# Kernel optimization log

Hardware: AMD Instinct MI355X
Metric: run time of the kernel (lower is better)

The kernel has to match this reference:

```python
import jax, jax.numpy as jnp
import numpy as np

N_STATE = 512   # n
N_CTRL = 128    # m
HORIZON = 256   # T


def setup_inputs() -> dict:
    key = jax.random.key(0)
    k1, k2, k3, k4 = jax.random.split(key, 4)
    dim = N_STATE + N_CTRL
    # F scaled for a stable backward Riccati recursion over HORIZON steps
    F = jax.random.normal(k1, (N_STATE, dim), jnp.float32) * (0.3 / np.sqrt(dim))
    f = jax.random.normal(k2, (N_STATE,), jnp.float32) * 0.1
    # SPD cost matrix so Q_uu is always invertible (positive definite)
    A = jax.random.normal(k3, (dim, dim), jnp.float32)
    C = A @ A.T / dim + jnp.eye(dim, dtype=jnp.float32)
    c = jax.random.normal(k4, (dim,), jnp.float32) * 0.1
    return {"F": F, "f": f, "C": C, "c": c, "T": HORIZON}


def reference(F, f, C, c, T):
    n = F.shape[0]  # state size
    # final value function: V = C_xx, v = c_x, const = 0
    V0 = C[:n, :n]
    v0 = c[:n]
    const0 = jnp.zeros((), C.dtype)

    def step(carry, _):
        V, v, const = carry
        # compute_Q
        FV = F.T @ V                 # [(n+m), n]
        Q = C + FV @ F               # [(n+m), (n+m)]
        q = c + FV @ f + F.T @ v     # [(n+m)]
        Quu = Q[n:, n:]
        Qux = Q[n:, :n]
        qu = q[n:]
        # compute_K
        inv_Quu = jnp.linalg.inv(Quu)
        K = -inv_Quu @ Qux           # [m, n]
        k = -inv_Quu @ qu            # [m]
        # compute_V
        Qxx = Q[:n, :n]
        Qxu = Q[:n, n:]
        qx = q[:n]
        KQuu = K.T @ Quu
        Vn = Qxx + Qxu @ K + K.T @ Qux + KQuu @ K
        vn = qx + Qxu @ k + K.T @ qu + KQuu @ k
        # compute_const (note: W in compute_W equals Q algebraically, so W_uu=Quu, w_u=qu)
        Vf = V @ f
        constn = const + 0.5 * (k @ (Quu @ k)) + k @ qu + 0.5 * (f @ Vf) + f @ v
        return (Vn, vn, constn), (K, k, Vn, vn, constn)

    _, ys = jax.lax.scan(step, (V0, v0, const0), None, length=T)
    Ks, ks, Vs, vs, consts = ys
    # original inserts at front each iteration -> reverse time axis;
    # value_fn[:-1] drops the final (terminal) V, i.e. keeps exactly the T step outputs
    rev = lambda a: a[::-1]
    return (rev(Ks), rev(ks), rev(Vs), rev(vs), rev(consts))
```

## Files before the change

### kernel.cpp

```cpp
#include <hip/hip_runtime.h>
#include <math.h>

#define N_ST 512
#define N_CT 128
#define DIM  640
#define T_H  256
#define LTRI 8256

__global__ __launch_bounds__(256) void gemm_tn(
    const float* __restrict__ A, int lda,
    const float* __restrict__ B, int ldb,
    const float* __restrict__ Cs, int ldc,
    float* __restrict__ D, int ldd,
    int K, float alpha)
{
  __shared__ float As[16][34];
  __shared__ float Bs[16][68];
  const int tid = threadIdx.x;
  const int tx = tid & 15, ty = tid >> 4;
  const int i0 = blockIdx.x * 32, j0 = blockIdx.y * 64;
  const int iiA = tid & 31, kkA = tid >> 5;
  const int jjB = tid & 63, kkB = tid >> 6;
  float acc[2][4] = {};
  for (int k0 = 0; k0 < K; k0 += 16) {
    As[kkA][iiA]   = A[(size_t)(k0 + kkA) * lda + i0 + iiA];
    As[kkA+8][iiA] = A[(size_t)(k0 + kkA + 8) * lda + i0 + iiA];
#pragma unroll
    for (int r = 0; r < 4; r++)
      Bs[kkB + 4*r][jjB] = B[(size_t)(k0 + kkB + 4*r) * ldb + j0 + jjB];
    __syncthreads();
#pragma unroll
    for (int kk = 0; kk < 16; kk++) {
      float a0 = As[kk][ty*2+0], a1 = As[kk][ty*2+1];
      float b0 = Bs[kk][tx*4+0], b1 = Bs[kk][tx*4+1];
      float b2 = Bs[kk][tx*4+2], b3 = Bs[kk][tx*4+3];
      acc[0][0] += a0*b0; acc[0][1] += a0*b1; acc[0][2] += a0*b2; acc[0][3] += a0*b3;
      acc[1][0] += a1*b0; acc[1][1] += a1*b1; acc[1][2] += a1*b2; acc[1][3] += a1*b3;
    }
    __syncthreads();
  }
#pragma unroll
  for (int r = 0; r < 2; r++) {
    int i = i0 + ty*2 + r, j = j0 + tx*4;
    float4 o;
    o.x = alpha*acc[r][0]; o.y = alpha*acc[r][1];
    o.z = alpha*acc[r][2]; o.w = alpha*acc[r][3];
    if (Cs) {
      float4 c4 = *(const float4*)(Cs + (size_t)i*ldc + j);
      o.x += c4.x; o.y += c4.y; o.z += c4.z; o.w += c4.w;
    }
    *(float4*)(D + (size_t)i*ldd + j) = o;
  }
}

__global__ __launch_bounds__(256) void gemm_nn(
    const float* __restrict__ A, int lda,
    const float* __restrict__ B, int ldb,
    const float* __restrict__ Cs, int ldc,
    float* __restrict__ D, int ldd,
    int K)
{
  __shared__ float As[32][17];
  __shared__ float Bs[16][68];
  const int tid = threadIdx.x;
  const int tx = tid & 15, ty = tid >> 4;
  const int i0 = blockIdx.x * 32, j0 = blockIdx.y * 64;
  const int kkA = tid & 15, iiA = tid >> 4;
  const int jjB = tid & 63, kkB = tid >> 6;
  float acc[2][4] = {};
  for (int k0 = 0; k0 < K; k0 += 16) {
    As[iiA][kkA]     = A[(size_t)(i0 + iiA) * lda + k0 + kkA];
    As[iiA+16][kkA]  = A[(size_t)(i0 + iiA + 16) * lda + k0 + kkA];
#pragma unroll
    for (int r = 0; r < 4; r++)
      Bs[kkB + 4*r][jjB] = B[(size_t)(k0 + kkB + 4*r) * ldb + j0 + jjB];
    __syncthreads();
#pragma unroll
    for (int kk = 0; kk < 16; kk++) {
      float a0 = As[ty*2+0][kk], a1 = As[ty*2+1][kk];
      float b0 = Bs[kk][tx*4+0], b1 = Bs[kk][tx*4+1];
      float b2 = Bs[kk][tx*4+2], b3 = Bs[kk][tx*4+3];
      acc[0][0] += a0*b0; acc[0][1] += a0*b1; acc[0][2] += a0*b2; acc[0][3] += a0*b3;
      acc[1][0] += a1*b0; acc[1][1] += a1*b1; acc[1][2] += a1*b2; acc[1][3] += a1*b3;
    }
    __syncthreads();
  }
#pragma unroll
  for (int r = 0; r < 2; r++) {
    int i = i0 + ty*2 + r, j = j0 + tx*4;
    float4 c4 = *(const float4*)(Cs + (size_t)i*ldc + j);
    float4 o;
    o.x = c4.x + acc[r][0]; o.y = c4.y + acc[r][1];
    o.z = c4.z + acc[r][2]; o.w = c4.w + acc[r][3];
    *(float4*)(D + (size_t)i*ldd + j) = o;
  }
}

__global__ __launch_bounds__(1024) void combo_kernel(
    const float* __restrict__ Qm,
    const float* __restrict__ FV,
    const float* __restrict__ F,
    const float* __restrict__ f,
    const float* __restrict__ cvec,
    const float* __restrict__ vin,
    const float* __restrict__ Vin, int ldV,
    float* __restrict__ qv,
    float* __restrict__ Vf,
    float* __restrict__ fv,
    float* __restrict__ Lout,
    float* __restrict__ invd)
{
  __shared__ float Sp[LTRI];
  __shared__ float dinv[128];
  __shared__ float red[1024];
  const int tid = threadIdx.x;
  const int b = blockIdx.x;

  if (b == 0) {
    for (int idx = tid; idx < LTRI; idx += 1024) {
      int r = (int)((sqrtf(8.0f*idx + 1.0f) - 1.0f) * 0.5f);
      while ((r+1)*(r+2)/2 <= idx) r++;
      while (r*(r+1)/2 > idx) r--;
      int c = idx - r*(r+1)/2;
      Sp[idx] = Qm[(size_t)(N_ST + r)*DIM + N_ST + c];
    }
    __syncthreads();

    for (int p = 0; p < 128; p += 16) {
      if (tid < 64) {
        const int t = tid;
        const int toff = (p + t)*(p + t + 1)/2;
        float a[16];
#pragma unroll
        for (int c2 = 0; c2 < 16; c2++)
          a[c2] = (t < 16 && c2 <= t) ? Sp[toff + p + c2] : 0.0f;
        float Lr[16];
        float myinv = 0.0f;
#pragma unroll
        for (int j = 0; j < 16; j++) {
          float dj  = __shfl(a[j], j);
          float sq  = sqrtf(dj);
          float inv = 1.0f / sq;
          float Ltj = (t == j) ? sq : a[j] * inv;
#pragma unroll
          for (int jp = j + 1; jp < 16; jp++) {
            float Lpj = __shfl(Ltj, jp);
            a[jp] -= Ltj * Lpj;
          }
          Lr[j] = Ltj;
          if (t == j) myinv = inv;
        }
        if (t < 16) {
#pragma unroll
          for (int j = 0; j < 16; j++)
            if (j <= t) Sp[toff + p + j] = Lr[j];
          dinv[p + t] = myinv;
        }
      }
      __syncthreads();

      {
        int r = p + 16 + tid;
        if (r < 128) {
          const int roff = r*(r+1)/2;
          float Lrow[16];
#pragma unroll
          for (int jj = 0; jj < 16; jj++) {
            float accv = Sp[roff + p + jj];
            const int doff = (p + jj)*(p + jj + 1)/2;
#pragma unroll
            for (int t2 = 0; t2 < 16; t2++)
              if (t2 < jj) accv -= Lrow[t2] * Sp[doff + p + t2];
            Lrow[jj] = accv * dinv[p + jj];
          }
#pragma unroll
          for (int jj = 0; jj < 16; jj++) Sp[roff + p + jj] = Lrow[jj];
        }
      }
      __syncthreads();

      {
        int nR = 112 - p;
        if (nR > 0) {
          int nq = nR >> 2;
          int pairs = nq * (nq + 1) / 2;
          for (int e = tid; e < pairs; e += 1024) {
            int ri = (int)((sqrtf(8.0f*e + 1.0f) - 1.0f) * 0.5f);
            while ((ri+1)*(ri+2)/2 <= e) ri++;
            while (ri*(ri+1)/2 > e) ri--;
            int ci = e - ri*(ri+1)/2;
            int r0 = p + 16 + ri*4;
            int c0 = p + 16 + ci*4;
            bool dg = (ri == ci);
            int ro[4], co[4];
#pragma unroll
            for (int i2 = 0; i2 < 4; i2++) ro[i2] = (r0+i2)*(r0+i2+1)/2;
#pragma unroll
            for (int j2 = 0; j2 < 4; j2++) co[j2] = (c0+j2)*(c0+j2+1)/2;
            float acc[4][4];
#pragma unroll
            for (int i2 = 0; i2 < 4; i2++)
#pragma unroll
              for (int j2 = 0; j2 < 4; j2++)
                acc[i2][j2] = (!dg || (c0+j2) <= (r0+i2)) ? Sp[ro[i2] + c0 + j2] : 0.0f;
#pragma unroll
            for (int t2 = 0; t2 < 16; t2++) {
              float rv[4], cv2[4];
#pragma unroll
              for (int i2 = 0; i2 < 4; i2++) rv[i2]  = Sp[ro[i2] + p + t2];
#pragma unroll
              for (int j2 = 0; j2 < 4; j2++) cv2[j2] = Sp[co[j2] + p + t2];
#pragma unroll
              for (int i2 = 0; i2 < 4; i2++)
#pragma unroll
                for (int j2 = 0; j2 < 4; j2++)
                  acc[i2][j2] -= rv[i2] * cv2[j2];
            }
#pragma unroll
            for (int i2 = 0; i2 < 4; i2++)
#pragma unroll
              for (int j2 = 0; j2 < 4; j2++)
                if (!dg || (c0+j2) <= (r0+i2)) Sp[ro[i2] + c0 + j2] = acc[i2][j2];
          }
        }
      }
      __syncthreads();
    }

    for (int idx = tid; idx < LTRI; idx += 1024) Lout[idx] = Sp[idx];
    if (tid < 128) invd[tid] = dinv[tid];

  } else if (b == 1) {
    if (tid < DIM) {
      float acc = cvec[tid];
      const float4* fr = (const float4*)(FV + (size_t)tid * N_ST);
      const float4* f4 = (const float4*)f;
      float a4 = 0.0f;
      for (int kk = 0; kk < N_ST/4; kk++) {
        float4 x = fr[kk], y = f4[kk];
        a4 += x.x*y.x + x.y*y.y + x.z*y.z + x.w*y.w;
      }
      float a2 = 0.0f;
      for (int k = 0; k < N_ST; k++)
        a2 += F[(size_t)k*DIM + tid] * vin[k];
      qv[tid] = acc + a4 + a2;
    }
  } else {
    if (tid < N_ST) {
      const float4* vr = (const float4*)(Vin + (size_t)tid * ldV);
      const float4* f4 = (const float4*)f;
      float a4 = 0.0f;
      for (int kk = 0; kk < N_ST/4; kk++) {
        float4 x = vr[kk], y = f4[kk];
        a4 += x.x*y.x + x.y*y.y + x.z*y.z + x.w*y.w;
      }
      Vf[tid] = a4;
    }
    float pv = (tid < N_ST) ? f[tid] * vin[tid] : 0.0f;
    red[tid] = pv;
    __syncthreads();
    for (int s2 = 512; s2 > 0; s2 >>= 1) {
      if (tid < s2) red[tid] += red[tid + s2];
      __syncthreads();
    }
    if (tid == 0) *fv = red[0];
  }
}

__global__ __launch_bounds__(256) void trsm_kernel(
    const float* __restrict__ Lw,
    const float* __restrict__ invd,
    const float* __restrict__ Qm,
    const float* __restrict__ qv,
    float* __restrict__ W,
    float* __restrict__ wv,
    float* __restrict__ kv,
    float* __restrict__ outK,
    float* __restrict__ outks)
{
  __shared__ float Lp[LTRI];
  __shared__ float di[128];
  const int tid = threadIdx.x;
  for (int idx = tid; idx < LTRI; idx += 256) Lp[idx] = Lw[idx];
  if (tid < 128) di[tid] = invd[tid];
  __syncthreads();

  const int wvid = tid >> 6, lane = tid & 63;
  const int j = blockIdx.x * 4 + wvid;
  if (j > N_ST) return;

  float b0, b1;
  if (j < N_ST) {
    b0 = Qm[(size_t)(N_ST + lane)*DIM + j];
    b1 = Qm[(size_t)(N_ST + 64 + lane)*DIM + j];
  } else {
    b0 = qv[N_ST + lane];
    b1 = qv[N_ST + 64 + lane];
  }

  float x0 = 0.0f, x1 = 0.0f;
  int uoff = 0;
  for (int u = 0; u < 128; u++) {
    float s = Lp[uoff + lane]*x0 + Lp[uoff + 64 + lane]*x1;
#pragma unroll
    for (int off = 32; off > 0; off >>= 1) s += __shfl_xor(s, off);
    float bu = (u < 64) ? __shfl(b0, u) : __shfl(b1, u - 64);
    float wu = (bu - s) * di[u];
    if (u < 64) { if (lane == u)      x0 = wu; }
    else        { if (lane == u - 64) x1 = wu; }
    uoff += u + 1;
  }
  if (j < N_ST) {
    W[(size_t)lane*N_ST + j]        = x0;
    W[(size_t)(64 + lane)*N_ST + j] = x1;
  } else {
    wv[lane] = x0; wv[64 + lane] = x1;
  }

  const int toff0 = lane*(lane + 1)/2;
  const int toff1 = (64 + lane)*(65 + lane)/2;
  float y0 = 0.0f, y1 = 0.0f;
  for (int u = 127; u >= 0; u--) {
    float s = Lp[toff0 + u]*y0 + Lp[toff1 + u]*y1;
#pragma unroll
    for (int off = 32; off > 0; off >>= 1) s += __shfl_xor(s, off);
    float wu2 = (u < 64) ? __shfl(x0, u) : __shfl(x1, u - 64);
    float yu = (wu2 - s) * di[u];
    if (u < 64) { if (lane == u)      y0 = yu; }
    else        { if (lane == u - 64) y1 = yu; }
  }
  if (j < N_ST) {
    outK[(size_t)lane*N_ST + j]        = -y0;
    outK[(size_t)(64 + lane)*N_ST + j] = -y1;
  } else {
    kv[lane] = -y0; kv[64 + lane] = -y1;
    outks[lane] = -y0; outks[64 + lane] = -y1;
  }
}

__global__ __launch_bounds__(256) void finish_kernel(
    const float* __restrict__ Qm,
    const float* __restrict__ qv,
    const float* __restrict__ W,
    const float* __restrict__ wv,
    const float* __restrict__ kv,
    const float* __restrict__ Vf,
    const float* __restrict__ fv,
    const float* __restrict__ f,
    const float* __restrict__ constp,
    float* __restrict__ outV,
    float* __restrict__ outv,
    float* __restrict__ outc,
    float* __restrict__ wsconst)
{
  const int b = blockIdx.x, tid = threadIdx.x;
  if (b < 128) {
    __shared__ float As[16][34];
    __shared__ float Bs[16][68];
    const int tx = tid & 15, ty = tid >> 4;
    const int i0 = (b >> 3) * 32, j0 = (b & 7) * 64;
    const int iiA = tid & 31, kkA = tid >> 5;
    const int jjB = tid & 63, kkB = tid >> 6;
    float acc[2][4] = {};
    for (int k0 = 0; k0 < N_CT; k0 += 16) {
      As[kkA][iiA]   = W[(size_t)(k0 + kkA)*N_ST + i0 + iiA];
      As[kkA+8][iiA] = W[(size_t)(k0 + kkA + 8)*N_ST + i0 + iiA];
#pragma unroll
      for (int r = 0; r < 4; r++)
        Bs[kkB + 4*r][jjB] = W[(size_t)(k0 + kkB + 4*r)*N_ST + j0 + jjB];
      __syncthreads();
#pragma unroll
      for (int kk = 0; kk < 16; kk++) {
        float a0 = As[kk][ty*2+0], a1 = As[kk][ty*2+1];
        float b0v = Bs[kk][tx*4+0], b1v = Bs[kk][tx*4+1];
        float b2v = Bs[kk][tx*4+2], b3v = Bs[kk][tx*4+3];
        acc[0][0] += a0*b0v; acc[0][1] += a0*b1v; acc[0][2] += a0*b2v; acc[0][3] += a0*b3v;
        acc[1][0] += a1*b0v; acc[1][1] += a1*b1v; acc[1][2] += a1*b2v; acc[1][3] += a1*b3v;
      }
      __syncthreads();
    }
#pragma unroll
    for (int r = 0; r < 2; r++) {
      int i = i0 + ty*2 + r, j = j0 + tx*4;
      float4 qx = *(const float4*)(Qm + (size_t)i*DIM + j);
      float4 o;
      o.x = qx.x - acc[r][0]; o.y = qx.y - acc[r][1];
      o.z = qx.z - acc[r][2]; o.w = qx.w - acc[r][3];
      *(float4*)(outV + (size_t)i*N_ST + j) = o;
    }
  } else if (b < 136) {
    if (tid < 64) {
      int i = (b - 128)*64 + tid;
      float acc = 0.0f;
      for (int u = 0; u < N_CT; u++) acc += W[(size_t)u*N_ST + i] * wv[u];
      outv[i] = qv[i] - acc;
    }
  } else {
    __shared__ float red[256];
    float pv = 0.0f;
    if (tid < 128) {
      float qk = 0.0f;
      for (int u = 0; u < 128; u++)
        qk += Qm[(size_t)(N_ST + tid)*DIM + N_ST + u] * kv[u];
      pv = kv[tid] * (0.5f*qk + qv[N_ST + tid]);
      float fa = 0.0f;
#pragma unroll
      for (int r = 0; r < 4; r++) { int jj = tid*4 + r; fa += f[jj] * Vf[jj]; }
      pv += 0.5f * fa;
    }
    red[tid] = pv;
    __syncthreads();
    for (int s2 = 128; s2 > 0; s2 >>= 1) {
      if (tid < s2) red[tid] += red[tid + s2];
      __syncthreads();
    }
    if (tid == 0) {
      float cn = constp[0] + red[0] + fv[0];
      outc[0] = cn;
      wsconst[0] = cn;
    }
  }
}

extern "C" void kernel_launch(void* const* d_in, const int* in_sizes, int n_in,
                              void* d_out, int out_size, void* d_ws, size_t ws_size,
                              hipStream_t stream)
{
  (void)in_sizes; (void)n_in; (void)out_size; (void)ws_size;
  const float* F  = (const float*)d_in[0];
  const float* f  = (const float*)d_in[1];
  const float* Cm = (const float*)d_in[2];
  const float* cv = (const float*)d_in[3];

  float* out   = (float*)d_out;
  float* outK  = out;
  float* outks = outK  + (size_t)T_H * N_CT * N_ST;
  float* outVs = outks + (size_t)T_H * N_CT;
  float* outvs = outVs + (size_t)T_H * N_ST * N_ST;
  float* outcs = outvs + (size_t)T_H * N_ST;

  float* ws   = (float*)d_ws;
  float* FV   = ws;
  float* Qm   = FV   + (size_t)DIM * N_ST;
  float* qv   = Qm   + (size_t)DIM * DIM;
  float* Lw   = qv   + DIM;
  float* invd = Lw   + LTRI;
  float* W    = invd + N_CT;
  float* wv   = W    + (size_t)N_CT * N_ST;
  float* kv   = wv   + N_CT;
  float* Vf   = kv   + N_CT;
  float* fv   = Vf   + N_ST;
  float* cst  = fv   + 1;

  hipMemsetAsync(cst, 0, sizeof(float), stream);

  for (int s = 0; s < T_H; s++) {
    const float* Vin; int ldV; const float* vin;
    if (s == 0) { Vin = Cm; ldV = DIM; vin = cv; }
    else {
      Vin = outVs + (size_t)(T_H - s) * N_ST * N_ST; ldV = N_ST;
      vin = outvs + (size_t)(T_H - s) * N_ST;
    }
    const size_t slot = (size_t)(T_H - 1 - s);

    dim3 g1(DIM/32, N_ST/64);
    gemm_tn<<<g1, 256, 0, stream>>>(F, DIM, Vin, ldV, nullptr, 0, FV, N_ST,
                                    N_ST, 1.0f);
    dim3 g2(DIM/32, DIM/64);
    gemm_nn<<<g2, 256, 0, stream>>>(FV, N_ST, F, DIM, Cm, DIM, Qm, DIM, N_ST);
    combo_kernel<<<3, 1024, 0, stream>>>(Qm, FV, F, f, cv, vin, Vin, ldV,
                                         qv, Vf, fv, Lw, invd);
    trsm_kernel<<<129, 256, 0, stream>>>(Lw, invd, Qm, qv, W, wv, kv,
                                         outK + slot * N_CT * N_ST,
                                         outks + slot * N_CT);
    finish_kernel<<<137, 256, 0, stream>>>(Qm, qv, W, wv, kv, Vf, fv, f, cst,
                                           outVs + slot * N_ST * N_ST,
                                           outvs + slot * N_ST,
                                           outcs + slot, cst);
  }
}
```

Before: 56.59 ms.

## Use split-bf16 MFMA GEMMs for Riccati matrix products

Replaces the scalar FP32 tiled GEMMs (F^T V, FV F, and the V update W^T W) with one MFMA kernel. It emulates fp32 using a bf16 hi/lo split and three bf16 MFMAs per tile product. F^T is converted once up front, and each GEMM epilogue emits the bf16 hi/lo copies the next step consumes. W is now stored transposed so the update and the vector matvec read contiguous rows. Dropping the lo*lo term and using bf16 pieces may cost some accuracy over the 256-step recursion.

```diff
diff --git a/kernel.cpp b/kernel.cpp
--- a/kernel.cpp
+++ b/kernel.cpp
@@ -7,93 +7,120 @@
 #define T_H  256
 #define LTRI 8256
 
-__global__ __launch_bounds__(256) void gemm_tn(
-    const float* __restrict__ A, int lda,
-    const float* __restrict__ B, int ldb,
-    const float* __restrict__ Cs, int ldc,
+typedef __attribute__((ext_vector_type(8))) short bf16x8;
+typedef __attribute__((ext_vector_type(4))) float f32x4;
+
+__device__ __forceinline__ ushort f2bf(float x) {
+  unsigned u = __float_as_uint(x);
+  unsigned r = (u + 0x7fffu + ((u >> 16) & 1u)) >> 16;
+  return (ushort)r;
+}
+__device__ __forceinline__ float bf2f(ushort h) {
+  return __uint_as_float(((unsigned)h) << 16);
+}
+
+__global__ __launch_bounds__(256) void gemm_nt_mfma(
+    const ushort* __restrict__ Ah, const ushort* __restrict__ Al, int lda,
+    const ushort* __restrict__ Bh, const ushort* __restrict__ Bl, int ldb,
+    const float* __restrict__ Cs, int ldc, float beta,
     float* __restrict__ D, int ldd,
-    int K, float alpha)
-{
-  __shared__ float As[16][34];
-  __shared__ float Bs[16][68];
+    ushort* __restrict__ Dh, ushort* __restrict__ Dl,
+    int K)
+{
+  __shared__ ushort As_h[64*72], As_l[64*72], Bs_h[64*72], Bs_l[64*72];
   const int tid = threadIdx.x;
-  const int tx = tid & 15, ty = tid >> 4;
-  const int i0 = blockIdx.x * 32, j0 = blockIdx.y * 64;
-  const int iiA = tid & 31, kkA = tid >> 5;
-  const int jjB = tid & 63, kkB = tid >> 6;
-  float acc[2][4] = {};
-  for (int k0 = 0; k0 < K; k0 += 16) {
-    As[kkA][iiA]   = A[(size_t)(k0 + kkA) * lda + i0 + iiA];
-    As[kkA+8][iiA] = A[(size_t)(k0 + kkA + 8) * lda + i0 + iiA];
-#pragma unroll
-    for (int r = 0; r < 4; r++)
-      Bs[kkB + 4*r][jjB] = B[(size_t)(k0 + kkB + 4*r) * ldb + j0 + jjB];
+  const int i0 = blockIdx.x * 64, j0 = blockIdx.y * 64;
+  const int wid = tid >> 6, lane = tid & 63;
+  const int wm = (wid & 1) * 32, wn = (wid >> 1) * 32;
+  const int fr = lane & 15, fq = lane >> 4;
+
+  f32x4 acc[2][2];
+#pragma unroll
+  for (int a = 0; a < 2; a++)
+#pragma unroll
+    for (int b = 0; b < 2; b++) acc[a][b] = (f32x4){0.f, 0.f, 0.f, 0.f};
+
+  for (int k0 = 0; k0 < K; k0 += 64) {
+#pragma unroll
+    for (int h = 0; h < 2; h++) {
+      int c = tid + h * 256;
+      int row = c >> 3, col = (c & 7) << 3;
+      *(uint4*)&As_h[row*72 + col] = *(const uint4*)&Ah[(size_t)(i0+row)*lda + k0 + col];
+      *(uint4*)&As_l[row*72 + col] = *(const uint4*)&Al[(size_t)(i0+row)*lda + k0 + col];
+      *(uint4*)&Bs_h[row*72 + col] = *(const uint4*)&Bh[(size_t)(j0+row)*ldb + k0 + col];
+      *(uint4*)&Bs_l[row*72 + col] = *(const uint4*)&Bl[(size_t)(j0+row)*ldb + k0 + col];
+    }
     __syncthreads();
 #pragma unroll
-    for (int kk = 0; kk < 16; kk++) {
-      float a0 = As[kk][ty*2+0], a1 = As[kk][ty*2+1];
-      float b0 = Bs[kk][tx*4+0], b1 = Bs[kk][tx*4+1];
-      float b2 = Bs[kk][tx*4+2], b3 = Bs[kk][tx*4+3];
-      acc[0][0] += a0*b0; acc[0][1] += a0*b1; acc[0][2] += a0*b2; acc[0][3] += a0*b3;
-      acc[1][0] += a1*b0; acc[1][1] += a1*b1; acc[1][2] += a1*b2; acc[1][3] += a1*b3;
+    for (int kc = 0; kc < 64; kc += 32) {
+      bf16x8 ah[2], al[2], bh[2], bl[2];
+#pragma unroll
+      for (int t = 0; t < 2; t++) {
+        ah[t] = *(bf16x8*)&As_h[(wm + t*16 + fr)*72 + kc + fq*8];
+        al[t] = *(bf16x8*)&As_l[(wm + t*16 + fr)*72 + kc + fq*8];
+        bh[t] = *(bf16x8*)&Bs_h[(wn + t*16 + fr)*72 + kc + fq*8];
+        bl[t] = *(bf16x8*)&Bs_l[(wn + t*16 + fr)*72 + kc + fq*8];
+      }
+#pragma unroll
+      for (int tm = 0; tm < 2; tm++)
+#pragma unroll
+        for (int tn = 0; tn < 2; tn++) {
+          acc[tm][tn] = __builtin_amdgcn_mfma_f32_16x16x32_bf16(ah[tm], bh[tn], acc[tm][tn], 0, 0, 0);
+          acc[tm][tn] = __builtin_amdgcn_mfma_f32_16x16x32_bf16(ah[tm], bl[tn], acc[tm][tn], 0, 0, 0);
+          acc[tm][tn] = __builtin_amdgcn_mfma_f32_16x16x32_bf16(al[tm], bh[tn], acc[tm][tn], 0, 0, 0);
+        }
     }
     __syncthreads();
   }
-#pragma unroll
-  for (int r = 0; r < 2; r++) {
-    int i = i0 + ty*2 + r, j = j0 + tx*4;
-    float4 o;
-    o.x = alpha*acc[r][0]; o.y = alpha*acc[r][1];
-    o.z = alpha*acc[r][2]; o.w = alpha*acc[r][3];
-    if (Cs) {
-      float4 c4 = *(const float4*)(Cs + (size_t)i*ldc + j);
-      o.x += c4.x; o.y += c4.y; o.z += c4.z; o.w += c4.w;
-    }
-    *(float4*)(D + (size_t)i*ldd + j) = o;
-  }
-}
-
-__global__ __launch_bounds__(256) void gemm_nn(
-    const float* __restrict__ A, int lda,
-    const float* __restrict__ B, int ldb,
-    const float* __restrict__ Cs, int ldc,
-    float* __restrict__ D, int ldd,
-    int K)
-{
-  __shared__ float As[32][17];
-  __shared__ float Bs[16][68];
-  const int tid = threadIdx.x;
-  const int tx = tid & 15, ty = tid >> 4;
-  const int i0 = blockIdx.x * 32, j0 = blockIdx.y * 64;
-  const int kkA = tid & 15, iiA = tid >> 4;
-  const int jjB = tid & 63, kkB = tid >> 6;
-  float acc[2][4] = {};
-  for (int k0 = 0; k0 < K; k0 += 16) {
-    As[iiA][kkA]     = A[(size_t)(i0 + iiA) * lda + k0 + kkA];
-    As[iiA+16][kkA]  = A[(size_t)(i0 + iiA + 16) * lda + k0 + kkA];
-#pragma unroll
-    for (int r = 0; r < 4; r++)
-      Bs[kkB + 4*r][jjB] = B[(size_t)(k0 + kkB + 4*r) * ldb + j0 + jjB];
-    __syncthreads();
-#pragma unroll
-    for (int kk = 0; kk < 16; kk++) {
-      float a0 = As[ty*2+0][kk], a1 = As[ty*2+1][kk];
-      float b0 = Bs[kk][tx*4+0], b1 = Bs[kk][tx*4+1];
-      float b2 = Bs[kk][tx*4+2], b3 = Bs[kk][tx*4+3];
-      acc[0][0] += a0*b0; acc[0][1] += a0*b1; acc[0][2] += a0*b2; acc[0][3] += a0*b3;
-      acc[1][0] += a1*b0; acc[1][1] += a1*b1; acc[1][2] += a1*b2; acc[1][3] += a1*b3;
-    }
-    __syncthreads();
-  }
-#pragma unroll
-  for (int r = 0; r < 2; r++) {
-    int i = i0 + ty*2 + r, j = j0 + tx*4;
-    float4 c4 = *(const float4*)(Cs + (size_t)i*ldc + j);
-    float4 o;
-    o.x = c4.x + acc[r][0]; o.y = c4.y + acc[r][1];
-    o.z = c4.z + acc[r][2]; o.w = c4.w + acc[r][3];
-    *(float4*)(D + (size_t)i*ldd + j) = o;
-  }
+
+#pragma unroll
+  for (int tm = 0; tm < 2; tm++)
+#pragma unroll
+    for (int tn = 0; tn < 2; tn++)
+#pragma unroll
+      for (int r = 0; r < 4; r++) {
+        int i = i0 + wm + tm*16 + fq*4 + r;
+        int j = j0 + wn + tn*16 + fr;
+        float v = beta * acc[tm][tn][r];
+        if (Cs) v += Cs[(size_t)i*ldc + j];
+        D[(size_t)i*ldd + j] = v;
+        if (Dh) {
+          ushort h = f2bf(v);
+          Dh[(size_t)i*ldd + j] = h;
+          Dl[(size_t)i*ldd + j] = f2bf(v - bf2f(h));
+        }
+      }
+}
+
+__global__ __launch_bounds__(256) void convert_FT(
+    const float* __restrict__ F, ushort* __restrict__ FTh, ushort* __restrict__ FTl)
+{
+  __shared__ float tile[32][33];
+  const int bi = blockIdx.x, bk = blockIdx.y;
+  const int tx = threadIdx.x & 31, ty = threadIdx.x >> 5;
+#pragma unroll
+  for (int r = 0; r < 4; r++)
+    tile[ty + r*8][tx] = F[(size_t)(bk*32 + ty + r*8)*DIM + bi*32 + tx];
+  __syncthreads();
+#pragma unroll
+  for (int r = 0; r < 4; r++) {
+    float v = tile[tx][ty + r*8];
+    ushort h = f2bf(v);
+    size_t o = (size_t)(bi*32 + ty + r*8)*N_ST + bk*32 + tx;
+    FTh[o] = h;
+    FTl[o] = f2bf(v - bf2f(h));
+  }
+}
+
+__global__ __launch_bounds__(256) void convert_V0(
+    const float* __restrict__ Cm, ushort* __restrict__ Vh, ushort* __restrict__ Vl)
+{
+  int idx = blockIdx.x * 256 + threadIdx.x;
+  int i = idx >> 9, j = idx & 511;
+  float v = Cm[(size_t)i*DIM + j];
+  ushort h = f2bf(v);
+  Vh[(size_t)i*N_ST + j] = h;
+  Vl[(size_t)i*N_ST + j] = f2bf(v - bf2f(h));
 }
 
 __global__ __launch_bounds__(1024) void combo_kernel(
@@ -272,7 +299,9 @@
     const float* __restrict__ invd,
     const float* __restrict__ Qm,
     const float* __restrict__ qv,
-    float* __restrict__ W,
+    float* __restrict__ Wt,
+    ushort* __restrict__ Wth,
+    ushort* __restrict__ Wtl,
     float* __restrict__ wv,
     float* __restrict__ kv,
     float* __restrict__ outK,
@@ -311,8 +340,11 @@
     uoff += u + 1;
   }
   if (j < N_ST) {
-    W[(size_t)lane*N_ST + j]        = x0;
-    W[(size_t)(64 + lane)*N_ST + j] = x1;
+    size_t o = (size_t)j * N_CT;
+    Wt[o + lane] = x0; Wt[o + 64 + lane] = x1;
+    ushort h0 = f2bf(x0), h1 = f2bf(x1);
+    Wth[o + lane] = h0;      Wtl[o + lane] = f2bf(x0 - bf2f(h0));
+    Wth[o + 64 + lane] = h1; Wtl[o + 64 + lane] = f2bf(x1 - bf2f(h1));
   } else {
     wv[lane] = x0; wv[64 + lane] = x1;
   }
@@ -338,63 +370,31 @@
   }
 }
 
-__global__ __launch_bounds__(256) void finish_kernel(
+__global__ __launch_bounds__(256) void finish_aux(
     const float* __restrict__ Qm,
     const float* __restrict__ qv,
-    const float* __restrict__ W,
+    const float* __restrict__ Wt,
     const float* __restrict__ wv,
     const float* __restrict__ kv,
     const float* __restrict__ Vf,
     const float* __restrict__ fv,
     const float* __restrict__ f,
     const float* __restrict__ constp,
-    float* __restrict__ outV,
     float* __restrict__ outv,
     float* __restrict__ outc,
     float* __restrict__ wsconst)
 {
   const int b = blockIdx.x, tid = threadIdx.x;
-  if (b < 128) {
-    __shared__ float As[16][34];
-    __shared__ float Bs[16][68];
-    const int tx = tid & 15, ty = tid >> 4;
-    const int i0 = (b >> 3) * 32, j0 = (b & 7) * 64;
-    const int iiA = tid & 31, kkA = tid >> 5;
-    const int jjB = tid & 63, kkB = tid >> 6;
-    float acc[2][4] = {};
-    for (int k0 = 0; k0 < N_CT; k0 += 16) {
-      As[kkA][iiA]   = W[(size_t)(k0 + kkA)*N_ST + i0 + iiA];
-      As[kkA+8][iiA] = W[(size_t)(k0 + kkA + 8)*N_ST + i0 + iiA];
-#pragma unroll
-      for (int r = 0; r < 4; r++)
-        Bs[kkB + 4*r][jjB] = W[(size_t)(k0 + kkB + 4*r)*N_ST + j0 + jjB];
-      __syncthreads();
-#pragma unroll
-      for (int kk = 0; kk < 16; kk++) {
-        float a0 = As[kk][ty*2+0], a1 = As[kk][ty*2+1];
-        float b0v = Bs[kk][tx*4+0], b1v = Bs[kk][tx*4+1];
-        float b2v = Bs[kk][tx*4+2], b3v = Bs[kk][tx*4+3];
-        acc[0][0] += a0*b0v; acc[0][1] += a0*b1v; acc[0][2] += a0*b2v; acc[0][3] += a0*b3v;
-        acc[1][0] += a1*b0v; acc[1][1] += a1*b1v; acc[1][2] += a1*b2v; acc[1][3] += a1*b3v;
-      }
-      __syncthreads();
-    }
-#pragma unroll
-    for (int r = 0; r < 2; r++) {
-      int i = i0 + ty*2 + r, j = j0 + tx*4;
-      float4 qx = *(const float4*)(Qm + (size_t)i*DIM + j);
-      float4 o;
-      o.x = qx.x - acc[r][0]; o.y = qx.y - acc[r][1];
-      o.z = qx.z - acc[r][2]; o.w = qx.w - acc[r][3];
-      *(float4*)(outV + (size_t)i*N_ST + j) = o;
-    }
-  } else if (b < 136) {
-    if (tid < 64) {
-      int i = (b - 128)*64 + tid;
-      float acc = 0.0f;
-      for (int u = 0; u < N_CT; u++) acc += W[(size_t)u*N_ST + i] * wv[u];
-      outv[i] = qv[i] - acc;
-    }
+  if (b < 2) {
+    int i = b*256 + tid;
+    const float4* wr = (const float4*)(Wt + (size_t)i * N_CT);
+    const float4* w4 = (const float4*)wv;
+    float acc = 0.0f;
+    for (int u = 0; u < N_CT/4; u++) {
+      float4 x = wr[u], y = w4[u];
+      acc += x.x*y.x + x.y*y.y + x.z*y.z + x.w*y.w;
+    }
+    outv[i] = qv[i] - acc;
   } else {
     __shared__ float red[256];
     float pv = 0.0f;
@@ -445,14 +445,25 @@
   float* qv   = Qm   + (size_t)DIM * DIM;
   float* Lw   = qv   + DIM;
   float* invd = Lw   + LTRI;
-  float* W    = invd + N_CT;
-  float* wv   = W    + (size_t)N_CT * N_ST;
-  float* kv   = wv   + N_CT;
-  float* Vf   = kv   + N_CT;
+  float* Wt   = invd + 128;
+  float* wv   = Wt   + (size_t)N_ST * N_CT;
+  float* kv   = wv   + 128;
+  float* Vf   = kv   + 128;
   float* fv   = Vf   + N_ST;
-  float* cst  = fv   + 1;
+  float* cst  = fv   + 64;
+  ushort* FTh = (ushort*)(cst + 64);
+  ushort* FTl = FTh + (size_t)DIM * N_ST;
+  ushort* Vh  = FTl + (size_t)DIM * N_ST;
+  ushort* Vl  = Vh  + (size_t)N_ST * N_ST;
+  ushort* FVh = Vl  + (size_t)N_ST * N_ST;
+  ushort* FVl = FVh + (size_t)DIM * N_ST;
+  ushort* Wth = FVl + (size_t)DIM * N_ST;
+  ushort* Wtl = Wth + (size_t)N_ST * N_CT;
 
   hipMemsetAsync(cst, 0, sizeof(float), stream);
+
+  convert_FT<<<dim3(DIM/32, N_ST/32), 256, 0, stream>>>(F, FTh, FTl);
+  convert_V0<<<(N_ST*N_ST)/256, 256, 0, stream>>>(Cm, Vh, Vl);
 
   for (int s = 0; s < T_H; s++) {
     const float* Vin; int ldV; const float* vin;
@@ -463,19 +474,23 @@
     }
     const size_t slot = (size_t)(T_H - 1 - s);
 
-    dim3 g1(DIM/32, N_ST/64);
-    gemm_tn<<<g1, 256, 0, stream>>>(F, DIM, Vin, ldV, nullptr, 0, FV, N_ST,
-                                    N_ST, 1.0f);
-    dim3 g2(DIM/32, DIM/64);
-    gemm_nn<<<g2, 256, 0, stream>>>(FV, N_ST, F, DIM, Cm, DIM, Qm, DIM, N_ST);
+    gemm_nt_mfma<<<dim3(DIM/64, N_ST/64), 256, 0, stream>>>(
+        FTh, FTl, N_ST, Vh, Vl, N_ST, nullptr, 0, 1.0f,
+        FV, N_ST, FVh, FVl, N_ST);
+    gemm_nt_mfma<<<dim3(DIM/64, DIM/64), 256, 0, stream>>>(
+        FVh, FVl, N_ST, FTh, FTl, N_ST, Cm, DIM, 1.0f,
+        Qm, DIM, nullptr, nullptr, N_ST);
     combo_kernel<<<3, 1024, 0, stream>>>(Qm, FV, F, f, cv, vin, Vin, ldV,
                                          qv, Vf, fv, Lw, invd);
-    trsm_kernel<<<129, 256, 0, stream>>>(Lw, invd, Qm, qv, W, wv, kv,
+    trsm_kernel<<<129, 256, 0, stream>>>(Lw, invd, Qm, qv, Wt, Wth, Wtl,
+                                         wv, kv,
                                          outK + slot * N_CT * N_ST,
                                          outks + slot * N_CT);
-    finish_kernel<<<137, 256, 0, stream>>>(Qm, qv, W, wv, kv, Vf, fv, f, cst,
-                                           outVs + slot * N_ST * N_ST,
-                                           outvs + slot * N_ST,
-                                           outcs + slot, cst);
-  }
-}
+    gemm_nt_mfma<<<dim3(N_ST/64, N_ST/64), 256, 0, stream>>>(
+        Wth, Wtl, N_CT, Wth, Wtl, N_CT, Qm, DIM, -1.0f,
+        outVs + slot * N_ST * N_ST, N_ST, Vh, Vl, N_CT);
+    finish_aux<<<3, 256, 0, stream>>>(Qm, qv, Wt, wv, kv, Vf, fv, f, cst,
+                                      outvs + slot * N_ST,
+                                      outcs + slot, cst);
+  }
+}
```

New measurement: 50.05 ms. 1.13x faster.
